# Kernel tuning notes

Measured on AMD Instinct MI355X. Metric: run time of the kernel, lower is better.

The kernel has to match this reference:

```python
import jax, jax.numpy as jnp
import numpy as np

NUM_LAYER = 5
EMB = 256
N = 100000
E = 300000
SELF_LOOP_BOND = 4
BN_EPS = 1e-5


def setup_inputs() -> dict:
    key = jax.random.key(0)
    ks = jax.random.split(key, 16)
    f = lambda k, shape: jax.random.normal(k, shape, jnp.float32) * 0.02
    return {
        "x_atom": jax.random.randint(ks[0], (N,), 0, 120),
        "x_chir": jax.random.randint(ks[1], (N,), 0, 3),
        "edge_index": jax.random.randint(ks[2], (2, E), 0, N),
        "edge_bond": jax.random.randint(ks[3], (E,), 0, 4),
        "edge_dir": jax.random.randint(ks[4], (E,), 0, 3),
        "atom_emb": f(ks[5], (120, EMB)),
        "chir_emb": f(ks[6], (3, EMB)),
        "bond_embs": f(ks[7], (NUM_LAYER, 6, EMB)),
        "dir_embs": f(ks[8], (NUM_LAYER, 3, EMB)),
        "W1s": f(ks[9], (NUM_LAYER, 2 * EMB, EMB)),
        "b1s": f(ks[10], (NUM_LAYER, 2 * EMB)),
        "W2s": f(ks[11], (NUM_LAYER, EMB, 2 * EMB)),
        "b2s": f(ks[12], (NUM_LAYER, EMB)),
        "bn_w": jnp.ones((NUM_LAYER, EMB), jnp.float32),
        "bn_b": jnp.zeros((NUM_LAYER, EMB), jnp.float32),
    }


def reference(x_atom, x_chir, edge_index, edge_bond, edge_dir,
              atom_emb, chir_emb, bond_embs, dir_embs,
              W1s, b1s, W2s, b2s, bn_w, bn_b):
    n = x_atom.shape[0]
    src, dst = edge_index[0], edge_index[1]
    # add self loops (edge_attr = [4, 0] for each node)
    loop = jnp.arange(n)
    src_full = jnp.concatenate([src, loop])          # [E+N]
    dst_full = jnp.concatenate([dst, loop])          # [E+N]
    bond_full = jnp.concatenate([edge_bond, jnp.full((n,), SELF_LOOP_BOND, edge_bond.dtype)])
    dir_full = jnp.concatenate([edge_dir, jnp.zeros((n,), edge_dir.dtype)])

    # initial node features: atom + chirality embeddings
    h = atom_emb[x_atom] + chir_emb[x_chir]          # [N, EMB]

    for l in range(NUM_LAYER):
        # per-layer edge embeddings (bond type + bond direction)
        e_emb = bond_embs[l][bond_full] + dir_embs[l][dir_full]   # [E+N, EMB]
        # message = x_j + edge_attr; aggregate = scatter-add to dst
        msg = h[src_full] + e_emb                                  # gather
        agg = jax.ops.segment_sum(msg, dst_full, num_segments=n)  # scatter-add
        # update MLP: Linear(EMB->2EMB) -> ReLU -> Linear(2EMB->EMB)
        hmid = jax.nn.relu(agg @ W1s[l].T + b1s[l])                # [N, 2EMB]
        h2 = hmid @ W2s[l].T + b2s[l]                              # [N, EMB]
        # batch norm (training mode: batch statistics, biased variance)
        mean = h2.mean(axis=0)
        var = h2.var(axis=0)
        h2 = (h2 - mean) * jax.lax.rsqrt(var + BN_EPS) * bn_w[l] + bn_b[l]
        # relu on all but last layer; dropout with p=0 is identity
        if l < NUM_LAYER - 1:
            h2 = jax.nn.relu(h2)
        h = h2
    # JK == 'last'
    return h
```

## Files before the change

### kernel.cpp

```cpp
#include <hip/hip_runtime.h>

#define EMB 256
#define NLAYER 5
#define CHUNK 1024

typedef unsigned int u32;
typedef unsigned short u16;

typedef __bf16 bf16x8 __attribute__((ext_vector_type(8)));
typedef float f32x4 __attribute__((ext_vector_type(4)));

__device__ __forceinline__ float bf2f(u16 u) {
    union { u32 i; float f; } x; x.i = ((u32)u) << 16; return x.f;
}
__device__ __forceinline__ u16 f2bf(float f) {
    union { float f; u32 i; } x; x.f = f;
    u32 r = x.i + 0x7FFFu + ((x.i >> 16) & 1u);
    return (u16)(r >> 16);
}
__device__ __forceinline__ u32 cvt_pk_bf16(float lo, float hi) {
    u32 r;
    asm("v_cvt_pk_bf16_f32 %0, %1, %2" : "=v"(r) : "v"(lo), "v"(hi));
    return r;
}
__device__ __forceinline__ void unpack4(uint2 p, float* o) {
    union { u32 i; float f; } a, b, c, d;
    a.i = p.x << 16; b.i = p.x & 0xFFFF0000u;
    c.i = p.y << 16; d.i = p.y & 0xFFFF0000u;
    o[0] = a.f; o[1] = b.f; o[2] = c.f; o[3] = d.f;
}

#define GLOAD(dst, ptr) asm volatile("global_load_dwordx4 %0, %1, off" : "=&v"(dst) : "v"(ptr))
#define VMWAIT(n) asm volatile("s_waitcnt vmcnt(" #n ")" ::: "memory")

__global__ void k_detect(const u32* __restrict__ bnw_raw, int* __restrict__ flag) {
    if (threadIdx.x == 0 && blockIdx.x == 0)
        *flag = (bnw_raw[0] == 0x3F803F80u) ? 1 : 0;
}

struct Cvt { const void* s; u16* d; int n; };
struct CvtTab { Cvt t[10]; };

__global__ void k_convert(CvtTab tab, const int* __restrict__ flag, int maxn) {
    int f = *flag;
    int stride = gridDim.x * blockDim.x;
    for (int i = blockIdx.x * blockDim.x + threadIdx.x; i < maxn; i += stride) {
        for (int j = 0; j < 10; j++) {
            if (i < tab.t[j].n) {
                u16 v;
                if (f) v = ((const u16*)tab.t[j].s)[i];
                else   v = f2bf(((const float*)tab.t[j].s)[i]);
                tab.t[j].d[i] = v;
            }
        }
    }
}

__global__ void k_zero(u32* p, int n) {
    int i = blockIdx.x * blockDim.x + threadIdx.x;
    if (i < n) p[i] = 0u;
}

__global__ void k_hist(const int* __restrict__ eidx, const int* __restrict__ ebond,
                       const int* __restrict__ edir,
                       u32* __restrict__ cnt, u32* __restrict__ cntb, u32* __restrict__ cntd, int E) {
    int e = blockIdx.x * blockDim.x + threadIdx.x;
    if (e >= E) return;
    int dst = eidx[E + e];
    atomicAdd(&cnt[dst], 1u);
    atomicAdd(&cntb[dst * 4 + ebond[e]], 1u);
    atomicAdd(&cntd[dst * 3 + edir[e]], 1u);
}

__global__ void k_chunksum(const u32* __restrict__ cnt, u32* __restrict__ partial, int N) {
    int b = blockIdx.x, t = threadIdx.x;
    int base = b * CHUNK + t * 4;
    u32 s = 0;
    for (int i = 0; i < 4; i++) { int idx = base + i; if (idx < N) s += cnt[idx]; }
    __shared__ u32 red[256];
    red[t] = s; __syncthreads();
    for (int o = 128; o > 0; o >>= 1) { if (t < o) red[t] += red[t + o]; __syncthreads(); }
    if (t == 0) partial[b] = red[0];
}

__global__ void k_scanpartial(u32* partial, u32* indptr, int nch, int N) {
    if (threadIdx.x == 0 && blockIdx.x == 0) {
        u32 run = 0;
        for (int i = 0; i < nch; i++) { u32 x = partial[i]; partial[i] = run; run += x; }
        indptr[N] = run;
    }
}

__global__ void k_chunkscan(const u32* __restrict__ cnt, const u32* __restrict__ partial,
                            u32* __restrict__ indptr, u32* __restrict__ fillp, int N) {
    int b = blockIdx.x, t = threadIdx.x;
    int base = b * CHUNK + t * 4;
    u32 c[4]; u32 tsum = 0;
    for (int i = 0; i < 4; i++) { int idx = base + i; c[i] = (idx < N) ? cnt[idx] : 0u; tsum += c[i]; }
    __shared__ u32 sc[256];
    sc[t] = tsum; __syncthreads();
    for (int o = 1; o < 256; o <<= 1) {
        u32 x = (t >= o) ? sc[t - o] : 0u;
        __syncthreads();
        sc[t] += x;
        __syncthreads();
    }
    u32 run = partial[b] + sc[t] - tsum;
    for (int i = 0; i < 4; i++) {
        int idx = base + i;
        if (idx < N) { indptr[idx] = run; fillp[idx] = run; }
        run += c[i];
    }
}

__global__ void k_fill(const int* __restrict__ eidx, u32* __restrict__ fillp,
                       u32* __restrict__ srcs, int E) {
    int e = blockIdx.x * blockDim.x + threadIdx.x;
    if (e >= E) return;
    int dst = eidx[E + e];
    u32 pos = atomicAdd(&fillp[dst], 1u);
    srcs[pos] = (u32)eidx[e];
}

__global__ void k_h0(const int* __restrict__ xa, const int* __restrict__ xc,
                     const u16* __restrict__ aemb, const u16* __restrict__ cemb,
                     u16* __restrict__ H, int N) {
    int wave = threadIdx.x >> 6, lane = threadIdx.x & 63;
    int v = blockIdx.x * 4 + wave;
    if (v >= N) return;
    int a = xa[v], c = xc[v];
    int c4 = lane * 4;
    uint2 pa = *(const uint2*)(aemb + (size_t)a * EMB + c4);
    uint2 pc = *(const uint2*)(cemb + (size_t)c * EMB + c4);
    float fa[4], fc[4];
    unpack4(pa, fa); unpack4(pc, fc);
    ushort4 ov;
    ov.x = f2bf(fa[0] + fc[0]); ov.y = f2bf(fa[1] + fc[1]);
    ov.z = f2bf(fa[2] + fc[2]); ov.w = f2bf(fa[3] + fc[3]);
    *(ushort4*)(H + (size_t)v * EMB + c4) = ov;
}

__global__ void k_scatter(const u16* __restrict__ H, const u32* __restrict__ indptr,
                          const u32* __restrict__ srcs,
                          const u32* __restrict__ cntb, const u32* __restrict__ cntd,
                          const u16* __restrict__ bemb, const u16* __restrict__ demb,
                          const float* __restrict__ scsh, int relu,
                          u16* __restrict__ AGG, int N) {
    int wave = threadIdx.x >> 6, lane = threadIdx.x & 63;
    int v = blockIdx.x * 4 + wave;
    if (v >= N) return;
    int c4 = lane * 4;
    float sc[4] = {1.f, 1.f, 1.f, 1.f}, sh[4] = {0.f, 0.f, 0.f, 0.f};
    if (scsh) {
        float4 s0 = *(const float4*)(scsh + c4);
        float4 s1 = *(const float4*)(scsh + 256 + c4);
        sc[0] = s0.x; sc[1] = s0.y; sc[2] = s0.z; sc[3] = s0.w;
        sh[0] = s1.x; sh[1] = s1.y; sh[2] = s1.z; sh[3] = s1.w;
    }
    float acc[4] = {0.f, 0.f, 0.f, 0.f};
    u32 beg = indptr[v], end = indptr[v + 1];
    for (u32 e = beg; e < end; e++) {
        u32 s = srcs[e];
        uint2 p = *(const uint2*)(H + (size_t)s * EMB + c4);
        float f[4]; unpack4(p, f);
        for (int i = 0; i < 4; i++) {
            float y = f[i] * sc[i] + sh[i];
            if (relu) y = fmaxf(y, 0.f);
            acc[i] += y;
        }
    }
    {
        uint2 p = *(const uint2*)(H + (size_t)v * EMB + c4);
        float f[4]; unpack4(p, f);
        for (int i = 0; i < 4; i++) {
            float y = f[i] * sc[i] + sh[i];
            if (relu) y = fmaxf(y, 0.f);
            acc[i] += y;
        }
    }
    float cb[5];
    cb[0] = (float)cntb[v * 4 + 0]; cb[1] = (float)cntb[v * 4 + 1];
    cb[2] = (float)cntb[v * 4 + 2]; cb[3] = (float)cntb[v * 4 + 3]; cb[4] = 1.f;
    float cd[3];
    cd[0] = (float)cntd[v * 3 + 0] + 1.f; cd[1] = (float)cntd[v * 3 + 1]; cd[2] = (float)cntd[v * 3 + 2];
    for (int b = 0; b < 5; b++) {
        uint2 p = *(const uint2*)(bemb + b * EMB + c4);
        float f[4]; unpack4(p, f);
        for (int i = 0; i < 4; i++) acc[i] += cb[b] * f[i];
    }
    for (int d = 0; d < 3; d++) {
        uint2 p = *(const uint2*)(demb + d * EMB + c4);
        float f[4]; unpack4(p, f);
        for (int i = 0; i < 4; i++) acc[i] += cd[d] * f[i];
    }
    ushort4 ov;
    ov.x = f2bf(acc[0]); ov.y = f2bf(acc[1]); ov.z = f2bf(acc[2]); ov.w = f2bf(acc[3]);
    *(ushort4*)(AGG + (size_t)v * EMB + c4) = ov;
}

#define KP 264
#define HSS 272

#define G1STEP(BUF)                                                                              \
    {                                                                                            \
        _Pragma("unroll") for (int j = 0; j < 4; j++)                                            \
            _Pragma("unroll") for (int i = 0; i < 4; i++)                                        \
                acc1[i][j] = __builtin_amdgcn_mfma_f32_16x16x32_bf16(BUF[j], af[i], acc1[i][j], 0, 0, 0); \
        if (s + 3 < 8) {                                                                         \
            _Pragma("unroll") for (int j = 0; j < 4; j++)                                        \
                GLOAD(BUF[j], wp[j] + (s + 3) * 32);                                             \
        }                                                                                        \
    }

#define G2STEP(BUF)                                                                              \
    {                                                                                            \
        _Pragma("unroll") for (int i = 0; i < 4; i++)                                            \
            _Pragma("unroll") for (int j = 0; j < 4; j++)                                        \
                acc2[i][j] = __builtin_amdgcn_mfma_f32_16x16x32_bf16(hf[i], BUF[j], acc2[i][j], 0, 0, 0); \
        if (s + 3 < 8) {                                                                         \
            _Pragma("unroll") for (int j = 0; j < 4; j++)                                        \
                GLOAD(BUF[j], vp[j] + (s + 3) * 32);                                             \
        }                                                                                        \
    }

__global__ __launch_bounds__(256, 2) void k_fused(
    const u16* __restrict__ A, const u16* __restrict__ W1, const u16* __restrict__ b1,
    const u16* __restrict__ W2, const u16* __restrict__ b2,
    u16* __restrict__ C, float* __restrict__ S, int M) {
    __shared__ __align__(16) u16 As[64 * KP];
    __shared__ __align__(16) u16 Hs[64 * HSS];
    int m0 = blockIdx.x * 64;
    int t = threadIdx.x;
    int wave = t >> 6, lane = t & 63;
    int lr = lane & 15, quad = lane >> 4;
    int wq = wave * 64;

    for (int it = 0; it < 8; it++) {
        int ci = t + it * 256;
        int r = ci >> 5, kc = (ci & 31) * 8;
        int gr = m0 + r; if (gr > M - 1) gr = M - 1;
        *(uint4*)(As + r * KP + kc) = *(const uint4*)(A + (size_t)gr * 256 + kc);
    }

    f32x4 acc2[4][4];
    #pragma unroll
    for (int i = 0; i < 4; i++)
        #pragma unroll
        for (int j = 0; j < 4; j++)
            acc2[i][j] = (f32x4){0.f, 0.f, 0.f, 0.f};

    __syncthreads();

    #pragma unroll
    for (int nh = 0; nh < 2; nh++) {
        f32x4 acc1[4][4];
        #pragma unroll
        for (int i = 0; i < 4; i++)
            #pragma unroll
            for (int j = 0; j < 4; j++)
                acc1[i][j] = (f32x4){0.f, 0.f, 0.f, 0.f};
        const u16* W1h = W1 + (size_t)(nh * 256) * 256;
        const u16* wp[4];
        #pragma unroll
        for (int j = 0; j < 4; j++)
            wp[j] = W1h + (size_t)(wq + j * 16 + lr) * 256 + quad * 8;

        bf16x8 wbA[4], wbB[4], wbC[4];
        #pragma unroll
        for (int j = 0; j < 4; j++) GLOAD(wbA[j], wp[j] + 0);
        #pragma unroll
        for (int j = 0; j < 4; j++) GLOAD(wbB[j], wp[j] + 32);
        #pragma unroll
        for (int j = 0; j < 4; j++) GLOAD(wbC[j], wp[j] + 64);

        #pragma unroll
        for (int s = 0; s < 8; s++) {
            bf16x8 af[4];
            #pragma unroll
            for (int i = 0; i < 4; i++)
                af[i] = *(const bf16x8*)(As + (i * 16 + lr) * KP + s * 32 + quad * 8);
            if (s < 6) { VMWAIT(8); } else if (s == 6) { VMWAIT(4); } else { VMWAIT(0); }
            __builtin_amdgcn_sched_barrier(0);
            if (s % 3 == 0)      G1STEP(wbA)
            else if (s % 3 == 1) G1STEP(wbB)
            else                 G1STEP(wbC)
        }
        __syncthreads();
        #pragma unroll
        for (int j = 0; j < 4; j++) {
            int wl = wq + j * 16 + quad * 4;
            ushort4 bq = *(const ushort4*)(b1 + nh * 256 + wl);
            float bv0 = bf2f(bq.x), bv1 = bf2f(bq.y), bv2 = bf2f(bq.z), bv3 = bf2f(bq.w);
            #pragma unroll
            for (int i = 0; i < 4; i++) {
                float v0 = fmaxf(acc1[i][j][0] + bv0, 0.f);
                float v1 = fmaxf(acc1[i][j][1] + bv1, 0.f);
                float v2 = fmaxf(acc1[i][j][2] + bv2, 0.f);
                float v3 = fmaxf(acc1[i][j][3] + bv3, 0.f);
                uint2 ov;
                ov.x = cvt_pk_bf16(v0, v1);
                ov.y = cvt_pk_bf16(v2, v3);
                *(uint2*)(Hs + (i * 16 + lr) * HSS + wl) = ov;
            }
        }
        __syncthreads();
        const u16* W2h = W2 + nh * 256;
        const u16* vp[4];
        #pragma unroll
        for (int j = 0; j < 4; j++)
            vp[j] = W2h + (size_t)(wq + j * 16 + lr) * 512 + quad * 8;

        bf16x8 vbA[4], vbB[4], vbC[4];
        #pragma unroll
        for (int j = 0; j < 4; j++) GLOAD(vbA[j], vp[j] + 0);
        #pragma unroll
        for (int j = 0; j < 4; j++) GLOAD(vbB[j], vp[j] + 32);
        #pragma unroll
        for (int j = 0; j < 4; j++) GLOAD(vbC[j], vp[j] + 64);

        #pragma unroll
        for (int s = 0; s < 8; s++) {
            bf16x8 hf[4];
            #pragma unroll
            for (int i = 0; i < 4; i++)
                hf[i] = *(const bf16x8*)(Hs + (i * 16 + lr) * HSS + s * 32 + quad * 8);
            if (s < 6) { VMWAIT(8); } else if (s == 6) { VMWAIT(4); } else { VMWAIT(0); }
            __builtin_amdgcn_sched_barrier(0);
            if (s % 3 == 0)      G2STEP(vbA)
            else if (s % 3 == 1) G2STEP(vbB)
            else                 G2STEP(vbC)
        }
    }

    #pragma unroll
    for (int j = 0; j < 4; j++) {
        int gn = wq + j * 16 + lr;
        float bv = bf2f(b2[gn]);
        float s = 0.f, q = 0.f;
        #pragma unroll
        for (int i = 0; i < 4; i++) {
            int mbase = m0 + i * 16 + quad * 4;
            #pragma unroll
            for (int r = 0; r < 4; r++) {
                int gm = mbase + r;
                if (gm < M) {
                    float v = acc2[i][j][r] + bv;
                    C[(size_t)gm * 256 + gn] = f2bf(v);
                    s += v; q += v * v;
                }
            }
        }
        s += __shfl_xor(s, 16, 64); s += __shfl_xor(s, 32, 64);
        q += __shfl_xor(q, 16, 64); q += __shfl_xor(q, 32, 64);
        if (quad == 0) {
            atomicAdd(&S[gn], s);
            atomicAdd(&S[256 + gn], q);
        }
    }
}

__global__ void k_finalize(const float* __restrict__ S, const u16* __restrict__ bnw,
                           const u16* __restrict__ bnb, float* __restrict__ scsh, float invN) {
    int c = threadIdx.x;
    float mean = S[c] * invN;
    float var = S[256 + c] * invN - mean * mean;
    var = fmaxf(var, 0.f);
    float inv = rsqrtf(var + 1e-5f);
    float sc = bf2f(bnw[c]) * inv;
    scsh[c] = sc;
    scsh[256 + c] = bf2f(bnb[c]) - mean * sc;
}

__global__ void k_out(const u16* __restrict__ H2, const float* __restrict__ scsh,
                      void* __restrict__ out, const int* __restrict__ flag, int N) {
    int wave = threadIdx.x >> 6, lane = threadIdx.x & 63;
    int v = blockIdx.x * 4 + wave;
    if (v >= N) return;
    int c4 = lane * 4;
    float4 s0 = *(const float4*)(scsh + c4);
    float4 s1 = *(const float4*)(scsh + 256 + c4);
    uint2 p = *(const uint2*)(H2 + (size_t)v * EMB + c4);
    float f[4]; unpack4(p, f);
    float o0 = f[0] * s0.x + s1.x;
    float o1 = f[1] * s0.y + s1.y;
    float o2 = f[2] * s0.z + s1.z;
    float o3 = f[3] * s0.w + s1.w;
    if (*flag) {
        ushort4 ov;
        ov.x = f2bf(o0); ov.y = f2bf(o1); ov.z = f2bf(o2); ov.w = f2bf(o3);
        *(ushort4*)((u16*)out + (size_t)v * EMB + c4) = ov;
    } else {
        float4 ov = make_float4(o0, o1, o2, o3);
        *(float4*)((float*)out + (size_t)v * EMB + c4) = ov;
    }
}

extern "C" void kernel_launch(void* const* d_in, const int* in_sizes, int n_in,
                              void* d_out, int out_size, void* d_ws, size_t ws_size,
                              hipStream_t stream) {
    const int* x_atom = (const int*)d_in[0];
    const int* x_chir = (const int*)d_in[1];
    const int* eidx   = (const int*)d_in[2];
    const int* ebond  = (const int*)d_in[3];
    const int* edir   = (const int*)d_in[4];

    const int N = in_sizes[0];
    const int E = in_sizes[3];

    char* p = (char*)d_ws;
    size_t off = 0;
    auto alloc = [&](size_t bytes) -> void* {
        void* r = p + off;
        off += bytes;
        off = (off + 255) & ~(size_t)255;
        return r;
    };
    u16* X   = (u16*)alloc((size_t)N * EMB * 2);
    u16* Y   = (u16*)alloc((size_t)N * EMB * 2);
    u32* cz  = (u32*)alloc(((size_t)8 * N + NLAYER * 512) * 4);
    u32* cnt  = cz;
    u32* cntb = cz + N;
    u32* cntd = cz + 5 * (size_t)N;
    float* stats5 = (float*)(cz + 8 * (size_t)N);
    u32* indptr = (u32*)alloc((size_t)(N + 1) * 4);
    u32* fillp  = (u32*)alloc((size_t)N * 4);
    u32* srcs   = (u32*)alloc((size_t)E * 4);
    u32* partial = (u32*)alloc(256 * 4);
    float* scsh  = (float*)alloc(512 * 4);
    int* flag    = (int*)alloc(256);

    int csz[10] = {120 * EMB, 3 * EMB, NLAYER * 6 * EMB, NLAYER * 3 * EMB,
                   NLAYER * 512 * EMB, NLAYER * 512, NLAYER * EMB * 512, NLAYER * EMB,
                   NLAYER * EMB, NLAYER * EMB};
    u16* cbuf[10];
    for (int j = 0; j < 10; j++) cbuf[j] = (u16*)alloc((size_t)csz[j] * 2);
    u16* atom_emb  = cbuf[0];
    u16* chir_emb  = cbuf[1];
    u16* bond_embs = cbuf[2];
    u16* dir_embs  = cbuf[3];
    u16* W1s = cbuf[4];
    u16* b1s = cbuf[5];
    u16* W2s = cbuf[6];
    u16* b2s = cbuf[7];
    u16* bnw = cbuf[8];
    u16* bnb = cbuf[9];

    const int nodeBlocks = (N + 3) / 4;
    const int nch = (N + CHUNK - 1) / CHUNK;

    k_detect<<<1, 64, 0, stream>>>((const u32*)d_in[13], flag);
    {
        CvtTab tab;
        int maxn = 0;
        for (int j = 0; j < 10; j++) {
            tab.t[j].s = d_in[5 + j];
            tab.t[j].d = cbuf[j];
            tab.t[j].n = csz[j];
            if (csz[j] > maxn) maxn = csz[j];
        }
        k_convert<<<(maxn + 255) / 256, 256, 0, stream>>>(tab, flag, maxn);
    }

    {
        int z = 8 * N + NLAYER * 512;
        k_zero<<<(z + 255) / 256, 256, 0, stream>>>(cz, z);
    }
    k_hist<<<(E + 255) / 256, 256, 0, stream>>>(eidx, ebond, edir, cnt, cntb, cntd, E);
    k_chunksum<<<nch, 256, 0, stream>>>(cnt, partial, N);
    k_scanpartial<<<1, 64, 0, stream>>>(partial, indptr, nch, N);
    k_chunkscan<<<nch, 256, 0, stream>>>(cnt, partial, indptr, fillp, N);
    k_fill<<<(E + 255) / 256, 256, 0, stream>>>(eidx, fillp, srcs, E);

    k_h0<<<nodeBlocks, 256, 0, stream>>>(x_atom, x_chir, atom_emb, chir_emb, X, N);

    u16* H = X;
    u16* A = Y;
    const int mT64 = (N + 63) / 64;
    for (int l = 0; l < NLAYER; l++) {
        const u16* bemb = bond_embs + (size_t)l * 6 * EMB;
        const u16* demb = dir_embs + (size_t)l * 3 * EMB;
        const u16* W1 = W1s + (size_t)l * 512 * EMB;
        const u16* B1 = b1s + (size_t)l * 512;
        const u16* W2 = W2s + (size_t)l * EMB * 512;
        const u16* B2 = b2s + (size_t)l * EMB;
        float* stats = stats5 + (size_t)l * 512;

        k_scatter<<<nodeBlocks, 256, 0, stream>>>(H, indptr, srcs, cntb, cntd, bemb, demb,
                                                  (l == 0) ? nullptr : scsh, (l == 0) ? 0 : 1,
                                                  A, N);
        k_fused<<<mT64, 256, 0, stream>>>(A, W1, B1, W2, B2, A, stats, N);
        k_finalize<<<1, 256, 0, stream>>>(stats, bnw + (size_t)l * EMB, bnb + (size_t)l * EMB,
                                          scsh, 1.0f / (float)N);
        u16* tmp = H; H = A; A = tmp;
    }

    k_out<<<nodeBlocks, 256, 0, stream>>>(H, scsh, d_out, flag, N);
}
```

Measured before the change: 1.212 ms.

## Fuse neighbor aggregation into the MLP kernel and fold BN finalize inline

```diff
diff --git a/kernel.cpp b/kernel.cpp
--- a/kernel.cpp
+++ b/kernel.cpp
@@ -140,66 +140,18 @@
     *(ushort4*)(H + (size_t)v * EMB + c4) = ov;
 }
 
-__global__ void k_scatter(const u16* __restrict__ H, const u32* __restrict__ indptr,
-                          const u32* __restrict__ srcs,
-                          const u32* __restrict__ cntb, const u32* __restrict__ cntd,
-                          const u16* __restrict__ bemb, const u16* __restrict__ demb,
-                          const float* __restrict__ scsh, int relu,
-                          u16* __restrict__ AGG, int N) {
-    int wave = threadIdx.x >> 6, lane = threadIdx.x & 63;
-    int v = blockIdx.x * 4 + wave;
-    if (v >= N) return;
-    int c4 = lane * 4;
-    float sc[4] = {1.f, 1.f, 1.f, 1.f}, sh[4] = {0.f, 0.f, 0.f, 0.f};
-    if (scsh) {
-        float4 s0 = *(const float4*)(scsh + c4);
-        float4 s1 = *(const float4*)(scsh + 256 + c4);
-        sc[0] = s0.x; sc[1] = s0.y; sc[2] = s0.z; sc[3] = s0.w;
-        sh[0] = s1.x; sh[1] = s1.y; sh[2] = s1.z; sh[3] = s1.w;
-    }
-    float acc[4] = {0.f, 0.f, 0.f, 0.f};
-    u32 beg = indptr[v], end = indptr[v + 1];
-    for (u32 e = beg; e < end; e++) {
-        u32 s = srcs[e];
-        uint2 p = *(const uint2*)(H + (size_t)s * EMB + c4);
-        float f[4]; unpack4(p, f);
-        for (int i = 0; i < 4; i++) {
-            float y = f[i] * sc[i] + sh[i];
-            if (relu) y = fmaxf(y, 0.f);
-            acc[i] += y;
-        }
-    }
-    {
-        uint2 p = *(const uint2*)(H + (size_t)v * EMB + c4);
-        float f[4]; unpack4(p, f);
-        for (int i = 0; i < 4; i++) {
-            float y = f[i] * sc[i] + sh[i];
-            if (relu) y = fmaxf(y, 0.f);
-            acc[i] += y;
-        }
-    }
-    float cb[5];
-    cb[0] = (float)cntb[v * 4 + 0]; cb[1] = (float)cntb[v * 4 + 1];
-    cb[2] = (float)cntb[v * 4 + 2]; cb[3] = (float)cntb[v * 4 + 3]; cb[4] = 1.f;
-    float cd[3];
-    cd[0] = (float)cntd[v * 3 + 0] + 1.f; cd[1] = (float)cntd[v * 3 + 1]; cd[2] = (float)cntd[v * 3 + 2];
-    for (int b = 0; b < 5; b++) {
-        uint2 p = *(const uint2*)(bemb + b * EMB + c4);
-        float f[4]; unpack4(p, f);
-        for (int i = 0; i < 4; i++) acc[i] += cb[b] * f[i];
-    }
-    for (int d = 0; d < 3; d++) {
-        uint2 p = *(const uint2*)(demb + d * EMB + c4);
-        float f[4]; unpack4(p, f);
-        for (int i = 0; i < 4; i++) acc[i] += cd[d] * f[i];
-    }
-    ushort4 ov;
-    ov.x = f2bf(acc[0]); ov.y = f2bf(acc[1]); ov.z = f2bf(acc[2]); ov.w = f2bf(acc[3]);
-    *(ushort4*)(AGG + (size_t)v * EMB + c4) = ov;
-}
-
 #define KP 264
 #define HSS 272
+
+#define ACCROW(P)                                                     \
+    {                                                                 \
+        float f_[4]; unpack4(P, f_);                                  \
+        _Pragma("unroll") for (int k_ = 0; k_ < 4; k_++) {            \
+            float y_ = f_[k_] * sc[k_] + sh[k_];                      \
+            if (relu) y_ = fmaxf(y_, 0.f);                            \
+            acc[k_] += y_;                                            \
+        }                                                             \
+    }
 
 #define G1STEP(BUF)                                                                              \
     {                                                                                            \
@@ -224,7 +176,12 @@
     }
 
 __global__ __launch_bounds__(256, 2) void k_fused(
-    const u16* __restrict__ A, const u16* __restrict__ W1, const u16* __restrict__ b1,
+    const u16* __restrict__ H, const u32* __restrict__ indptr, const u32* __restrict__ srcs,
+    const u32* __restrict__ cntb, const u32* __restrict__ cntd,
+    const u16* __restrict__ bemb, const u16* __restrict__ demb,
+    const float* __restrict__ Sp, const u16* __restrict__ bnw, const u16* __restrict__ bnb,
+    float invN, int relu,
+    const u16* __restrict__ W1, const u16* __restrict__ b1,
     const u16* __restrict__ W2, const u16* __restrict__ b2,
     u16* __restrict__ C, float* __restrict__ S, int M) {
     __shared__ __align__(16) u16 As[64 * KP];
@@ -234,12 +191,77 @@
     int wave = t >> 6, lane = t & 63;
     int lr = lane & 15, quad = lane >> 4;
     int wq = wave * 64;
-
-    for (int it = 0; it < 8; it++) {
-        int ci = t + it * 256;
-        int r = ci >> 5, kc = (ci & 31) * 8;
-        int gr = m0 + r; if (gr > M - 1) gr = M - 1;
-        *(uint4*)(As + r * KP + kc) = *(const uint4*)(A + (size_t)gr * 256 + kc);
+    int c4 = lane * 4;
+
+    float sc[4] = {1.f, 1.f, 1.f, 1.f}, sh[4] = {0.f, 0.f, 0.f, 0.f};
+    if (Sp) {
+        float4 s0 = *(const float4*)(Sp + c4);
+        float4 s1 = *(const float4*)(Sp + 256 + c4);
+        ushort4 w4 = *(const ushort4*)(bnw + c4);
+        ushort4 b4 = *(const ushort4*)(bnb + c4);
+        float sv[4] = {s0.x, s0.y, s0.z, s0.w};
+        float qv[4] = {s1.x, s1.y, s1.z, s1.w};
+        u16 wv[4] = {w4.x, w4.y, w4.z, w4.w};
+        u16 bv[4] = {b4.x, b4.y, b4.z, b4.w};
+        #pragma unroll
+        for (int k = 0; k < 4; k++) {
+            float mean = sv[k] * invN;
+            float var = fmaxf(qv[k] * invN - mean * mean, 0.f);
+            float inv = rsqrtf(var + 1e-5f);
+            sc[k] = bf2f(wv[k]) * inv;
+            sh[k] = bf2f(bv[k]) - mean * sc[k];
+        }
+    }
+    float eb[8][4];
+    #pragma unroll
+    for (int b = 0; b < 5; b++) { uint2 p = *(const uint2*)(bemb + b * EMB + c4); unpack4(p, eb[b]); }
+    #pragma unroll
+    for (int d = 0; d < 3; d++) { uint2 p = *(const uint2*)(demb + d * EMB + c4); unpack4(p, eb[5 + d]); }
+
+    u32 nextbeg = 0;
+    {
+        int v0 = m0 + wave * 16;
+        if (v0 < M) nextbeg = indptr[v0];
+    }
+    #pragma unroll 1
+    for (int nn = 0; nn < 16; nn++) {
+        int r = wave * 16 + nn;
+        int v = m0 + r;
+        float acc[4] = {0.f, 0.f, 0.f, 0.f};
+        if (v < M) {
+            u32 beg = nextbeg;
+            u32 end = indptr[v + 1];
+            nextbeg = end;
+            uint2 pself = *(const uint2*)(H + (size_t)v * EMB + c4);
+            float cb0 = (float)cntb[v * 4 + 0], cb1 = (float)cntb[v * 4 + 1];
+            float cb2 = (float)cntb[v * 4 + 2], cb3 = (float)cntb[v * 4 + 3];
+            float cd0 = (float)cntd[v * 3 + 0] + 1.f;
+            float cd1 = (float)cntd[v * 3 + 1], cd2 = (float)cntd[v * 3 + 2];
+            u32 e = beg;
+            while (e < end) {
+                u32 rem = end - e;
+                u32 o1 = rem > 1 ? 1u : 0u, o2 = rem > 2 ? 2u : 0u, o3 = rem > 3 ? 3u : 0u;
+                u32 i0 = srcs[e], i1 = srcs[e + o1], i2 = srcs[e + o2], i3 = srcs[e + o3];
+                uint2 p0 = *(const uint2*)(H + (size_t)i0 * EMB + c4);
+                uint2 p1 = *(const uint2*)(H + (size_t)i1 * EMB + c4);
+                uint2 p2 = *(const uint2*)(H + (size_t)i2 * EMB + c4);
+                uint2 p3 = *(const uint2*)(H + (size_t)i3 * EMB + c4);
+                ACCROW(p0);
+                if (rem > 1) ACCROW(p1);
+                if (rem > 2) ACCROW(p2);
+                if (rem > 3) ACCROW(p3);
+                e += (rem < 4u) ? rem : 4u;
+            }
+            ACCROW(pself);
+            #pragma unroll
+            for (int k = 0; k < 4; k++)
+                acc[k] += cb0 * eb[0][k] + cb1 * eb[1][k] + cb2 * eb[2][k] + cb3 * eb[3][k] + eb[4][k]
+                        + cd0 * eb[5][k] + cd1 * eb[6][k] + cd2 * eb[7][k];
+        }
+        uint2 ov;
+        ov.x = cvt_pk_bf16(acc[0], acc[1]);
+        ov.y = cvt_pk_bf16(acc[2], acc[3]);
+        *(uint2*)(As + r * KP + c4) = ov;
     }
 
     f32x4 acc2[4][4];
@@ -359,32 +381,36 @@
     }
 }
 
-__global__ void k_finalize(const float* __restrict__ S, const u16* __restrict__ bnw,
-                           const u16* __restrict__ bnb, float* __restrict__ scsh, float invN) {
-    int c = threadIdx.x;
-    float mean = S[c] * invN;
-    float var = S[256 + c] * invN - mean * mean;
-    var = fmaxf(var, 0.f);
-    float inv = rsqrtf(var + 1e-5f);
-    float sc = bf2f(bnw[c]) * inv;
-    scsh[c] = sc;
-    scsh[256 + c] = bf2f(bnb[c]) - mean * sc;
-}
-
-__global__ void k_out(const u16* __restrict__ H2, const float* __restrict__ scsh,
+__global__ void k_out(const u16* __restrict__ H2, const float* __restrict__ Sp,
+                      const u16* __restrict__ bnw, const u16* __restrict__ bnb, float invN,
                       void* __restrict__ out, const int* __restrict__ flag, int N) {
     int wave = threadIdx.x >> 6, lane = threadIdx.x & 63;
     int v = blockIdx.x * 4 + wave;
     if (v >= N) return;
     int c4 = lane * 4;
-    float4 s0 = *(const float4*)(scsh + c4);
-    float4 s1 = *(const float4*)(scsh + 256 + c4);
+    float4 s0 = *(const float4*)(Sp + c4);
+    float4 s1 = *(const float4*)(Sp + 256 + c4);
+    ushort4 w4 = *(const ushort4*)(bnw + c4);
+    ushort4 b4 = *(const ushort4*)(bnb + c4);
+    float sv[4] = {s0.x, s0.y, s0.z, s0.w};
+    float qv[4] = {s1.x, s1.y, s1.z, s1.w};
+    u16 wv[4] = {w4.x, w4.y, w4.z, w4.w};
+    u16 bv[4] = {b4.x, b4.y, b4.z, b4.w};
+    float sc[4], sh[4];
+    #pragma unroll
+    for (int k = 0; k < 4; k++) {
+        float mean = sv[k] * invN;
+        float var = fmaxf(qv[k] * invN - mean * mean, 0.f);
+        float inv = rsqrtf(var + 1e-5f);
+        sc[k] = bf2f(wv[k]) * inv;
+        sh[k] = bf2f(bv[k]) - mean * sc[k];
+    }
     uint2 p = *(const uint2*)(H2 + (size_t)v * EMB + c4);
     float f[4]; unpack4(p, f);
-    float o0 = f[0] * s0.x + s1.x;
-    float o1 = f[1] * s0.y + s1.y;
-    float o2 = f[2] * s0.z + s1.z;
-    float o3 = f[3] * s0.w + s1.w;
+    float o0 = f[0] * sc[0] + sh[0];
+    float o1 = f[1] * sc[1] + sh[1];
+    float o2 = f[2] * sc[2] + sh[2];
+    float o3 = f[3] * sc[3] + sh[3];
     if (*flag) {
         ushort4 ov;
         ov.x = f2bf(o0); ov.y = f2bf(o1); ov.z = f2bf(o2); ov.w = f2bf(o3);
@@ -426,7 +452,6 @@
     u32* fillp  = (u32*)alloc((size_t)N * 4);
     u32* srcs   = (u32*)alloc((size_t)E * 4);
     u32* partial = (u32*)alloc(256 * 4);
-    float* scsh  = (float*)alloc(512 * 4);
     int* flag    = (int*)alloc(256);
 
     int csz[10] = {120 * EMB, 3 * EMB, NLAYER * 6 * EMB, NLAYER * 3 * EMB,
@@ -474,8 +499,9 @@
     k_h0<<<nodeBlocks, 256, 0, stream>>>(x_atom, x_chir, atom_emb, chir_emb, X, N);
 
     u16* H = X;
-    u16* A = Y;
+    u16* O = Y;
     const int mT64 = (N + 63) / 64;
+    const float invN = 1.0f / (float)N;
     for (int l = 0; l < NLAYER; l++) {
         const u16* bemb = bond_embs + (size_t)l * 6 * EMB;
         const u16* demb = dir_embs + (size_t)l * 3 * EMB;
@@ -484,15 +510,17 @@
         const u16* W2 = W2s + (size_t)l * EMB * 512;
         const u16* B2 = b2s + (size_t)l * EMB;
         float* stats = stats5 + (size_t)l * 512;
-
-        k_scatter<<<nodeBlocks, 256, 0, stream>>>(H, indptr, srcs, cntb, cntd, bemb, demb,
-                                                  (l == 0) ? nullptr : scsh, (l == 0) ? 0 : 1,
-                                                  A, N);
-        k_fused<<<mT64, 256, 0, stream>>>(A, W1, B1, W2, B2, A, stats, N);
-        k_finalize<<<1, 256, 0, stream>>>(stats, bnw + (size_t)l * EMB, bnb + (size_t)l * EMB,
-                                          scsh, 1.0f / (float)N);
-        u16* tmp = H; H = A; A = tmp;
-    }
-
-    k_out<<<nodeBlocks, 256, 0, stream>>>(H, scsh, d_out, flag, N);
-}
+        const float* Sprev = (l == 0) ? nullptr : stats5 + (size_t)(l - 1) * 512;
+        const u16* bw = bnw + (size_t)(l ? l - 1 : 0) * EMB;
+        const u16* bb = bnb + (size_t)(l ? l - 1 : 0) * EMB;
+
+        k_fused<<<mT64, 256, 0, stream>>>(H, indptr, srcs, cntb, cntd, bemb, demb,
+                                          Sprev, bw, bb, invN, (l == 0) ? 0 : 1,
+                                          W1, B1, W2, B2, O, stats, N);
+        u16* tmp = H; H = O; O = tmp;
+    }
+
+    k_out<<<nodeBlocks, 256, 0, stream>>>(H, stats5 + (size_t)4 * 512,
+                                          bnw + (size_t)4 * EMB, bnb + (size_t)4 * EMB, invN,
+                                          d_out, flag, N);
+}
```

After: 1.400 ms. +15.5%, slower.
